# Optimization experiments

Hardware: AMD Instinct MI355X
Metric: run time of the kernel (lower is better)

The kernel has to match this reference:

```python
import jax, jax.numpy as jnp
import numpy as np

TOL_CONTACT = 0.01  # contact tolerance from signed_dis


def _knn_pair(ref_pts, ref_nrm, q_pts, k):
    """Signed distance from each query point to the surface of one other object.

    ref_pts/ref_nrm: [Nr,3] reference object points (in plane frame) and normals.
    q_pts: [Nq,3] query object points (in plane frame). Returns [Nq].
    """
    # brute-force squared distances [Nq, Nr] (same math as tra.nearest_neighbor)
    sq = (jnp.sum(q_pts * q_pts, -1)[:, None]
          - 2.0 * (q_pts @ ref_pts.T)
          + jnp.sum(ref_pts * ref_pts, -1)[None, :])
    negd, idx = jax.lax.top_k(-sq, k)                  # k nearest per query: [Nq,k]
    dist = jnp.sqrt(jnp.maximum(-negd, 0.0))           # euclidean distances
    near = ref_pts[idx]                                # [Nq,k,3] gathered surface pts
    near_n = ref_nrm[idx]                              # [Nq,k,3] gathered normals
    grad = near - q_pts[:, None, :]
    grad = grad / jnp.linalg.norm(grad, axis=-1, keepdims=True)
    insides = jnp.sum(near_n * grad, axis=-1) > 0      # einsum('okij,okij->oki')
    inside = jnp.sum(insides, axis=-1) > k * 0.8       # majority vote over k
    # nearest-neighbor distance, sign-flipped when inside
    return jnp.where(inside, -dist[:, 0], dist[:, 0])


def reference(points, est_T, plane_T, k):
    M, N, _ = points.shape
    # transform object points into plane frame
    T = jnp.linalg.inv(plane_T)[None] @ est_T          # [M,4,4]
    xyz = points[..., :3]
    nrm = points[..., 3:6]
    pts_pl = jnp.einsum('mij,mnj->mni', T[:, :3, :3], xyz) + T[:, None, :3, 3]
    sd_plane = pts_pl[..., 2]                          # plane signed distance [M,N]

    # signed distance of object b's points to every other object o: pair[b,o,:]
    pair = jax.vmap(
        lambda q: jax.vmap(lambda rp, rn: _knn_pair(rp, rn, q, k))(pts_pl, nrm)
    )(pts_pl)                                          # [M,M,N]
    big = jnp.asarray(jnp.finfo(pair.dtype).max, pair.dtype)
    pair = jnp.where(jnp.eye(M, dtype=bool)[:, :, None], big, pair)
    sd_obj = jnp.min(pair, axis=1)                     # min over other objects [M,N]

    signed_distance = jnp.minimum(sd_plane, sd_obj)
    intersects = signed_distance < -TOL_CONTACT
    return signed_distance, intersects


def setup_inputs() -> dict:
    key = jax.random.key(0)
    kp, kn, kt, kpl = jax.random.split(key, 4)
    M, N = 4, 3072
    # objects offset from each other so pairwise nearest distances are > 0
    xyz = jax.random.normal(kp, (M, N, 3), jnp.float32) * 0.05 \
        + jnp.arange(M, dtype=jnp.float32)[:, None, None] * 0.3
    nrm = jax.random.normal(kn, (M, N, 3), jnp.float32)
    nrm = nrm / jnp.linalg.norm(nrm, axis=-1, keepdims=True)
    points = jnp.concatenate([xyz, nrm], axis=-1)      # [M,N,6]

    def rigid(k_, n):
        q, _ = jnp.linalg.qr(jax.random.normal(k_, (n, 3, 3), jnp.float32))
        t = jax.random.normal(jax.random.fold_in(k_, 7), (n, 3), jnp.float32) * 0.1
        T = jnp.zeros((n, 4, 4), jnp.float32)
        T = T.at[:, :3, :3].set(q).at[:, :3, 3].set(t).at[:, 3, 3].set(1.0)
        return T

    est_T = rigid(kt, M)        # per-object estimated transforms [M,4,4]
    plane_T = rigid(kpl, 1)[0]  # plane transform [4,4]
    return {"points": points, "est_T": est_T, "plane_T": plane_T, "k": 10}
```

## Files before the change

### kernel.cpp

```cpp
#include <hip/hip_runtime.h>
#include <math.h>

#define M_OBJ 4
#define N_PTS 3072
#define K_NN  10
#define NSLOT (M_OBJ - 1)
#define QPB   64
#define SEG   4
#define SEGN  (N_PTS / SEG)
#define NCHUNK (SEGN / 64)
#define WSTRIDE 16
#define NWARM (SEGN / WSTRIDE)

__device__ inline void make_T(const float* __restrict__ E,
                              const float* __restrict__ P,
                              float T[3][4]) {
    float Pi[3][4];
#pragma unroll
    for (int i = 0; i < 3; ++i) {
#pragma unroll
        for (int j = 0; j < 3; ++j) Pi[i][j] = P[j * 4 + i];
        Pi[i][3] = -(P[0 * 4 + i] * P[3] + P[1 * 4 + i] * P[7] + P[2 * 4 + i] * P[11]);
    }
#pragma unroll
    for (int i = 0; i < 3; ++i) {
#pragma unroll
        for (int j = 0; j < 4; ++j) {
            float acc = (j == 3) ? Pi[i][3] : 0.0f;
#pragma unroll
            for (int kk = 0; kk < 3; ++kk) acc += Pi[i][kk] * E[kk * 4 + j];
            T[i][j] = acc;
        }
    }
}

__device__ __forceinline__ void insertv(float v, float bs[K_NN]) {
#pragma unroll
    for (int i = 0; i < K_NN - 1; ++i)
        bs[i] = __builtin_amdgcn_fmed3f(v, bs[i], bs[i + 1]);
    bs[K_NN - 1] = fmaxf(v, bs[K_NN - 1]);
}

__global__ __launch_bounds__(256, 3) void pair_kernel(
        const float* __restrict__ points,
        const float* __restrict__ estT,
        const float* __restrict__ planeT,
        float* __restrict__ pair_sd) {
    __shared__ float4 sref[N_PTS];
    __shared__ float  mbuf[128 * K_NN];

    const int pidx  = blockIdx.x;
    const int q     = pidx / NSLOT;
    const int rs    = pidx % NSLOT;
    const int r     = rs + (rs >= q ? 1 : 0);
    const int tid   = threadIdx.x;
    const int seg   = tid >> 6;
    const int qlane = tid & 63;

    float Tq[3][4], Tr[3][4];
    make_T(estT + q * 16, planeT, Tq);
    make_T(estT + r * 16, planeT, Tr);

    for (int j = tid; j < N_PTS; j += 256) {
        const float* p = points + (size_t)(r * N_PTS + j) * 6;
        float2 xy = *(const float2*)p;
        float  z  = p[2];
        float px = Tr[0][0] * xy.x + Tr[0][1] * xy.y + Tr[0][2] * z + Tr[0][3];
        float py = Tr[1][0] * xy.x + Tr[1][1] * xy.y + Tr[1][2] * z + Tr[1][3];
        float pz = Tr[2][0] * xy.x + Tr[2][1] * xy.y + Tr[2][2] * z + Tr[2][3];
        float w  = 0.5f * (px * px + py * py + pz * pz);
        sref[j] = make_float4(px, py, pz, w);
    }
    __syncthreads();

    const int nq = blockIdx.y * QPB + qlane;
    const float* qp = points + (size_t)(q * N_PTS + nq) * 6;
    float2 qxy = *(const float2*)qp;
    float  qzz = qp[2];
    const float qx = Tq[0][0] * qxy.x + Tq[0][1] * qxy.y + Tq[0][2] * qzz + Tq[0][3];
    const float qy = Tq[1][0] * qxy.x + Tq[1][1] * qxy.y + Tq[1][2] * qzz + Tq[1][3];
    const float qz = Tq[2][0] * qxy.x + Tq[2][1] * qxy.y + Tq[2][2] * qzz + Tq[2][3];
    const float qq = qx * qx + qy * qy + qz * qz;

    const float* nrm_base = points + (size_t)r * N_PTS * 6 + 3;

    auto cand_packed = [&](int id) -> float {
        float4 p = sref[id];
        float s = fmaf(p.x, qx, fmaf(p.y, qy, fmaf(p.z, qz, -p.w)));
        const float* nb = nrm_base + (size_t)id * 6;
        float gx = p.x - qx, gy = p.y - qy, gz = p.z - qz;
        float dv = fmaf(nb[0], gx, fmaf(nb[1], gy, nb[2] * gz));
        unsigned su = (__float_as_uint(s) & ~1u) | (dv > 0.0f ? 1u : 0u);
        return __uint_as_float(su);
    };

    float bs[K_NN];
#pragma unroll
    for (int i = 0; i < K_NN; ++i) bs[i] = -3.4e38f;

    const int j0 = seg * SEGN;

#pragma unroll 4
    for (int t = 0; t < NWARM; ++t)
        insertv(cand_packed(j0 + t * WSTRIDE), bs);

    for (int c = 0; c < NCHUNK; ++c) {
        const int jj = j0 + c * 64;
        const float gate = __uint_as_float(__float_as_uint(bs[0]) & ~1u);
        unsigned w0 = 0u, w1 = 0u;
#pragma unroll
        for (int b = 0; b < 32; ++b) {
            float4 p = sref[jj + b];
            float s = fmaf(p.x, qx, fmaf(p.y, qy, fmaf(p.z, qz, -p.w)));
            w0 |= (s > gate) ? (1u << b) : 0u;
        }
#pragma unroll
        for (int b = 0; b < 32; ++b) {
            float4 p = sref[jj + 32 + b];
            float s = fmaf(p.x, qx, fmaf(p.y, qy, fmaf(p.z, qz, -p.w)));
            w1 |= (s > gate) ? (1u << b) : 0u;
        }
        w0 &= ~0x00010001u;
        w1 &= ~0x00010001u;

        while (__any((w0 | w1) != 0u)) {
            if (w0) {
                const int b = __builtin_ctz(w0); w0 &= w0 - 1u;
                insertv(cand_packed(jj + b), bs);
            }
            if (w1) {
                const int b = __builtin_ctz(w1); w1 &= w1 - 1u;
                insertv(cand_packed(jj + 32 + b), bs);
            }
        }
    }

    __syncthreads();
    if (seg >= 2) {
        const int slot = tid - 128;
#pragma unroll
        for (int i = 0; i < K_NN; ++i) mbuf[slot * K_NN + i] = bs[i];
    }
    __syncthreads();
    if (seg < 2) {
        const int src = (seg * 64 + qlane) * K_NN;
#pragma unroll
        for (int i = 0; i < K_NN; ++i) insertv(mbuf[src + i], bs);
    }
    __syncthreads();
    if (seg == 1) {
#pragma unroll
        for (int i = 0; i < K_NN; ++i) mbuf[qlane * K_NN + i] = bs[i];
    }
    __syncthreads();
    if (seg == 0) {
        const int src = qlane * K_NN;
#pragma unroll
        for (int i = 0; i < K_NN; ++i) insertv(mbuf[src + i], bs);

        int votes = 0;
#pragma unroll
        for (int i = 0; i < K_NN; ++i) votes += (__float_as_uint(bs[i]) & 1u);

        const float s1 = __uint_as_float(__float_as_uint(bs[K_NN - 1]) & ~1u);
        float sq = fmaxf(fmaf(-2.0f, s1, qq), 0.0f);
        float d0 = sqrtf(sq);
        float sd = (votes > 8) ? -d0 : d0;
        pair_sd[((size_t)q * NSLOT + rs) * N_PTS + nq] = sd;
    }
}

__global__ __launch_bounds__(256) void reduce_kernel(
        const float* __restrict__ points,
        const float* __restrict__ estT,
        const float* __restrict__ planeT,
        const float* __restrict__ pair_sd,
        float* __restrict__ out) {
    int i = blockIdx.x * blockDim.x + threadIdx.x;
    if (i >= M_OBJ * N_PTS) return;
    int m = i / N_PTS, n = i % N_PTS;

    float T[3][4];
    make_T(estT + m * 16, planeT, T);
    const float* p = points + (size_t)i * 6;
    float zpl = T[2][0] * p[0] + T[2][1] * p[1] + T[2][2] * p[2] + T[2][3];

    float sd = zpl;
#pragma unroll
    for (int rs = 0; rs < NSLOT; ++rs)
        sd = fminf(sd, pair_sd[((size_t)m * NSLOT + rs) * N_PTS + n]);

    out[i] = sd;
    out[M_OBJ * N_PTS + i] = (sd < -0.01f) ? 1.0f : 0.0f;
}

extern "C" void kernel_launch(void* const* d_in, const int* in_sizes, int n_in,
                              void* d_out, int out_size, void* d_ws, size_t ws_size,
                              hipStream_t stream) {
    const float* points = (const float*)d_in[0];
    const float* estT   = (const float*)d_in[1];
    const float* planeT = (const float*)d_in[2];

    float* pair_sd = (float*)d_ws;

    dim3 gridB(M_OBJ * NSLOT, N_PTS / QPB);
    pair_kernel<<<gridB, 256, 0, stream>>>(points, estT, planeT, pair_sd);

    int total = M_OBJ * N_PTS;
    reduce_kernel<<<(total + 255) / 256, 256, 0, stream>>>(points, estT, planeT,
                                                           pair_sd, (float*)d_out);
}
```

Before: 128.2 us.

## Pack neighbor index into score bits and defer normal-vote to final stage

Instead of computing the inside/outside normal dot product for every candidate inserted into the top-k list (with a global normal load each time), the 12 low mantissa bits of each score now carry the reference point index. Only after the merge are the k winners' normals fetched, their votes computed and the exact score recomputed. The selection gate is loosened slightly to account for the truncated mantissa. This removes global loads from the hot insertion path, at the cost of coarser score precision during selection, which could change neighbor ordering for near ties.

```diff
diff --git a/kernel.cpp b/kernel.cpp
--- a/kernel.cpp
+++ b/kernel.cpp
@@ -11,6 +11,8 @@
 #define NCHUNK (SEGN / 64)
 #define WSTRIDE 16
 #define NWARM (SEGN / WSTRIDE)
+#define IDBITS 12
+#define IDMASK ((1u << IDBITS) - 1u)
 
 __device__ inline void make_T(const float* __restrict__ E,
                               const float* __restrict__ P,
@@ -39,6 +41,10 @@
     for (int i = 0; i < K_NN - 1; ++i)
         bs[i] = __builtin_amdgcn_fmed3f(v, bs[i], bs[i + 1]);
     bs[K_NN - 1] = fmaxf(v, bs[K_NN - 1]);
+}
+
+__device__ __forceinline__ float score4(const float4 p, float qx, float qy, float qz) {
+    return fmaf(p.x, qx, fmaf(p.y, qy, fmaf(p.z, qz, -p.w)));
 }
 
 __global__ __launch_bounds__(256, 3) void pair_kernel(
@@ -82,16 +88,9 @@
     const float qz = Tq[2][0] * qxy.x + Tq[2][1] * qxy.y + Tq[2][2] * qzz + Tq[2][3];
     const float qq = qx * qx + qy * qy + qz * qz;
 
-    const float* nrm_base = points + (size_t)r * N_PTS * 6 + 3;
-
-    auto cand_packed = [&](int id) -> float {
-        float4 p = sref[id];
-        float s = fmaf(p.x, qx, fmaf(p.y, qy, fmaf(p.z, qz, -p.w)));
-        const float* nb = nrm_base + (size_t)id * 6;
-        float gx = p.x - qx, gy = p.y - qy, gz = p.z - qz;
-        float dv = fmaf(nb[0], gx, fmaf(nb[1], gy, nb[2] * gz));
-        unsigned su = (__float_as_uint(s) & ~1u) | (dv > 0.0f ? 1u : 0u);
-        return __uint_as_float(su);
+    auto pack = [&](int id) -> float {
+        float s = score4(sref[id], qx, qy, qz);
+        return __uint_as_float((__float_as_uint(s) & ~IDMASK) | (unsigned)id);
     };
 
     float bs[K_NN];
@@ -102,22 +101,21 @@
 
 #pragma unroll 4
     for (int t = 0; t < NWARM; ++t)
-        insertv(cand_packed(j0 + t * WSTRIDE), bs);
+        insertv(pack(j0 + t * WSTRIDE), bs);
 
     for (int c = 0; c < NCHUNK; ++c) {
         const int jj = j0 + c * 64;
-        const float gate = __uint_as_float(__float_as_uint(bs[0]) & ~1u);
+        const float b0 = bs[0];
+        const float gate = fmaf(-fabsf(b0), 1.0e-3f, b0) - 1e-30f;
         unsigned w0 = 0u, w1 = 0u;
 #pragma unroll
         for (int b = 0; b < 32; ++b) {
-            float4 p = sref[jj + b];
-            float s = fmaf(p.x, qx, fmaf(p.y, qy, fmaf(p.z, qz, -p.w)));
+            float s = score4(sref[jj + b], qx, qy, qz);
             w0 |= (s > gate) ? (1u << b) : 0u;
         }
 #pragma unroll
         for (int b = 0; b < 32; ++b) {
-            float4 p = sref[jj + 32 + b];
-            float s = fmaf(p.x, qx, fmaf(p.y, qy, fmaf(p.z, qz, -p.w)));
+            float s = score4(sref[jj + 32 + b], qx, qy, qz);
             w1 |= (s > gate) ? (1u << b) : 0u;
         }
         w0 &= ~0x00010001u;
@@ -126,11 +124,11 @@
         while (__any((w0 | w1) != 0u)) {
             if (w0) {
                 const int b = __builtin_ctz(w0); w0 &= w0 - 1u;
-                insertv(cand_packed(jj + b), bs);
+                insertv(pack(jj + b), bs);
             }
             if (w1) {
                 const int b = __builtin_ctz(w1); w1 &= w1 - 1u;
-                insertv(cand_packed(jj + 32 + b), bs);
+                insertv(pack(jj + 32 + b), bs);
             }
         }
     }
@@ -158,12 +156,21 @@
 #pragma unroll
         for (int i = 0; i < K_NN; ++i) insertv(mbuf[src + i], bs);
 
+        const float* nrm_base = points + (size_t)r * N_PTS * 6 + 3;
         int votes = 0;
-#pragma unroll
-        for (int i = 0; i < K_NN; ++i) votes += (__float_as_uint(bs[i]) & 1u);
-
-        const float s1 = __uint_as_float(__float_as_uint(bs[K_NN - 1]) & ~1u);
-        float sq = fmaxf(fmaf(-2.0f, s1, qq), 0.0f);
+        float s_best = -3.4e38f;
+#pragma unroll
+        for (int i = 0; i < K_NN; ++i) {
+            const int id = (int)(__float_as_uint(bs[i]) & IDMASK);
+            float4 p = sref[id];
+            float s = score4(p, qx, qy, qz);
+            if (i == K_NN - 1) s_best = s;
+            const float* nb = nrm_base + (size_t)id * 6;
+            float gx = p.x - qx, gy = p.y - qy, gz = p.z - qz;
+            votes += (fmaf(nb[0], gx, fmaf(nb[1], gy, nb[2] * gz)) > 0.0f) ? 1 : 0;
+        }
+
+        float sq = fmaxf(fmaf(-2.0f, s_best, qq), 0.0f);
         float d0 = sqrtf(sq);
         float sd = (votes > 8) ? -d0 : d0;
         pair_sd[((size_t)q * NSLOT + rs) * N_PTS + nq] = sd;
```

Result: faster. 119.7 us (-6.6%).
